# Performance work log

Measured on AMD Instinct MI355X. Metric: run time of the kernel, lower is better.

Reference implementation:

```python
import jax, jax.numpy as jnp
import numpy as np

C_IMG, C_TXT, NHEAD = 256, 768, 8
B, D, H, W, L = 8, 24, 24, 24, 77

def setup_inputs() -> dict:
    key = jax.random.key(0)
    ks = jax.random.split(key, 16)
    s = 0.02
    x_img = jax.random.normal(ks[0], (B, C_IMG, D, H, W), jnp.float32)
    x_txt = jax.random.normal(ks[1], (B, L, C_TXT), jnp.float32)
    # realistic padding: each sample has a valid length in [40, 77); True = padded key
    lengths = jax.random.randint(ks[2], (B,), 40, L)
    txt_mask = jnp.arange(L)[None, :] >= lengths[:, None]  # [B, L] bool
    inp = {
        "x_img": x_img,
        "x_txt": x_txt,
        "txt_mask": txt_mask,
        "q_proj_w": jax.random.normal(ks[3], (C_IMG, C_IMG), jnp.float32) * s,   # Conv3d 1x1, no bias
        "k_proj_w": jax.random.normal(ks[4], (C_IMG, C_TXT), jnp.float32) * s,   # Linear, no bias
        "v_proj_w": jax.random.normal(ks[5], (C_IMG, C_TXT), jnp.float32) * s,
        "in_q_w": jax.random.normal(ks[6], (C_IMG, C_IMG), jnp.float32) * s,     # MHA in_proj (q/k/v)
        "in_q_b": jnp.zeros((C_IMG,), jnp.float32),
        "in_k_w": jax.random.normal(ks[7], (C_IMG, C_IMG), jnp.float32) * s,
        "in_k_b": jnp.zeros((C_IMG,), jnp.float32),
        "in_v_w": jax.random.normal(ks[8], (C_IMG, C_IMG), jnp.float32) * s,
        "in_v_b": jnp.zeros((C_IMG,), jnp.float32),
        "out_proj_w": jax.random.normal(ks[9], (C_IMG, C_IMG), jnp.float32) * s, # MHA out_proj
        "out_proj_b": jnp.zeros((C_IMG,), jnp.float32),
        "out_conv_w": jax.random.normal(ks[10], (C_IMG, C_IMG), jnp.float32) * s, # self.out Conv3d 1x1 (bias)
        "out_conv_b": jnp.zeros((C_IMG,), jnp.float32),
        "norm_w": jnp.ones((C_IMG,), jnp.float32),  # InstanceNorm3d affine
        "norm_b": jnp.zeros((C_IMG,), jnp.float32),
    }
    return inp

def reference(x_img, x_txt, txt_mask, q_proj_w, k_proj_w, v_proj_w,
              in_q_w, in_q_b, in_k_w, in_k_b, in_v_w, in_v_b,
              out_proj_w, out_proj_b, out_conv_w, out_conv_b, norm_w, norm_b):
    Bq, C, d, h, w = x_img.shape
    N = d * h * w
    hd = C // NHEAD
    # q_proj (1x1 conv == channel matmul), flatten to tokens
    q = jnp.einsum('bcdhw,oc->bodhw', x_img, q_proj_w).reshape(Bq, C, N).transpose(0, 2, 1)  # [B,N,C]
    k = jnp.einsum('blt,ct->blc', x_txt, k_proj_w)  # [B,L,C]
    v = jnp.einsum('blt,ct->blc', x_txt, v_proj_w)
    # MHA internal projections
    qh = (q @ in_q_w.T + in_q_b).reshape(Bq, N, NHEAD, hd).transpose(0, 2, 1, 3)  # [B,h,N,hd]
    kh = (k @ in_k_w.T + in_k_b).reshape(Bq, -1, NHEAD, hd).transpose(0, 2, 1, 3)  # [B,h,L,hd]
    vh = (v @ in_v_w.T + in_v_b).reshape(Bq, -1, NHEAD, hd).transpose(0, 2, 1, 3)
    scores = jnp.einsum('bhnd,bhld->bhnl', qh, kh) / jnp.sqrt(jnp.asarray(hd, qh.dtype))
    neg = jnp.finfo(scores.dtype).min
    scores = jnp.where(txt_mask[:, None, None, :], neg, scores)
    attn = jax.nn.softmax(scores, axis=-1)  # [B,h,N,L]
    o = jnp.einsum('bhnl,bhld->bhnd', attn, vh).transpose(0, 2, 1, 3).reshape(Bq, N, C)
    o = o @ out_proj_w.T + out_proj_b
    o = o.transpose(0, 2, 1).reshape(Bq, C, d, h, w)
    # self.out 1x1 conv with bias
    o = jnp.einsum('bcdhw,oc->bodhw', o, out_conv_w) + out_conv_b[None, :, None, None, None]
    # residual + InstanceNorm3d(affine) + SiLU
    r = o + x_img
    mu = r.mean(axis=(2, 3, 4), keepdims=True)
    var = r.var(axis=(2, 3, 4), keepdims=True)
    xn = (r - mu) * jax.lax.rsqrt(var + 1e-5)
    out = jax.nn.silu(xn * norm_w[None, :, None, None, None] + norm_b[None, :, None, None, None])
    return out
```

## Files before the change

kernel.cpp:

```cpp
#include <hip/hip_runtime.h>
#include <cstdint>
#include <cstddef>

#define B_    8
#define CI    256
#define NH    8
#define HD    32
#define LQ    77
#define LP    80
#define NSP   13824
#define NTILE 216
#define SCALE 0.17677669529663687f

typedef float    float4_ __attribute__((ext_vector_type(4)));
typedef _Float16 half4_  __attribute__((ext_vector_type(4)));

#define MFMA16(a,b,c) __builtin_amdgcn_mfma_f32_16x16x16f16((a),(b),(c),0,0,0)

#define OFF_WQP  0
#define OFF_WOP  32768
#define OFF_WKP  65536
#define OFF_WVP  163840
#define OFF_KP   262144
#define OFF_VP   344064
#define OFF_BO   425984
#define OFF_IQBS 426240
#define OFF_AM   426496
#define OFF_STAT 427136

__global__ __launch_bounds__(256) void prep_kernel(
    const float* __restrict__ opb, const float* __restrict__ ocw,
    const float* __restrict__ ocb, const float* __restrict__ iqb,
    const void*  __restrict__ mask_in, float* __restrict__ ws)
{
    int blk = blockIdx.x, tid = threadIdx.x;
    if (blk == 0) {
        float a = ocb[tid];
        const float* row = ocw + tid * 256;
        #pragma unroll 4
        for (int m = 0; m < 256; ++m) a = fmaf(row[m], opb[m], a);
        ws[OFF_BO + tid] = a;
        ws[OFF_IQBS + tid] = iqb[tid] * SCALE;
    } else if (blk == 1) {
        __shared__ int s_is8;
        if (tid == 0) s_is8 = 0;
        __syncthreads();
        const unsigned char* m8 = (const unsigned char*)mask_in;
        for (int i = tid; i < B_ * LQ; i += 256)
            if ((i & 3) && m8[i]) atomicExch(&s_is8, 1);
        __syncthreads();
        int is8 = s_is8;
        const int* mi = (const int*)mask_in;
        float* mo = ws + OFF_AM;
        for (int i = tid; i < B_ * LP; i += 256) {
            int b = i / LP, l = i % LP;
            int v = 1;
            if (l < LQ) v = is8 ? (int)m8[b * LQ + l] : mi[b * LQ + l];
            mo[i] = v ? -1e30f : 0.0f;
        }
    } else {
        for (int i = tid; i < B_ * CI * 2; i += 256) ws[OFF_STAT + i] = 0.f;
    }
}

__global__ __launch_bounds__(256) void wcomb_kernel(
    const float* __restrict__ qpw, const float* __restrict__ iqw,
    const float* __restrict__ opw, const float* __restrict__ ocw,
    const float* __restrict__ kpw, const float* __restrict__ ikw,
    const float* __restrict__ vpw, const float* __restrict__ ivw,
    float* __restrict__ ws)
{
    int blk = blockIdx.x, tid = threadIdx.x;
    int lane = tid & 63, w = tid >> 6, g = lane >> 4, li = lane & 15;

    const float *iw, *pw; _Float16* dst; int pstride, ctb, otb; float scale = 1.f;
    if (blk < 16) {
        iw = iqw; pw = qpw; pstride = 256; dst = (_Float16*)(ws + OFF_WQP);
        ctb = blk >> 2; otb = blk & 3; scale = SCALE;
    } else if (blk < 32) {
        int j = blk - 16;
        iw = ocw; pw = opw; pstride = 256; dst = (_Float16*)(ws + OFF_WOP);
        ctb = j >> 2; otb = j & 3;
    } else if (blk < 80) {
        int j = blk - 32;
        iw = ikw; pw = kpw; pstride = 768; dst = (_Float16*)(ws + OFF_WKP);
        ctb = j >> 2; otb = j & 3;
    } else {
        int j = blk - 80;
        iw = ivw; pw = vpw; pstride = 768; dst = (_Float16*)(ws + OFF_WVP);
        ctb = j >> 2; otb = j & 3;
    }
    int ct = ctb * 4 + w;

    float4_ acc[4];
    #pragma unroll
    for (int i = 0; i < 4; ++i)
        #pragma unroll
        for (int r = 0; r < 4; ++r) acc[i][r] = 0.f;

    for (int mt = 0; mt < 16; ++mt) {
        half4_ ah;
        #pragma unroll
        for (int j = 0; j < 4; ++j)
            ah[j] = (_Float16)pw[(size_t)(mt * 16 + 4 * g + j) * pstride + ct * 16 + li];
        #pragma unroll
        for (int i = 0; i < 4; ++i) {
            int o = (otb * 4 + i) * 16 + li;
            float4_ bw = *(const float4_*)&iw[(size_t)o * 256 + mt * 16 + 4 * g];
            half4_ bh;
            #pragma unroll
            for (int j = 0; j < 4; ++j) bh[j] = (_Float16)bw[j];
            acc[i] = MFMA16(ah, bh, acc[i]);
        }
    }
    #pragma unroll
    for (int i = 0; i < 4; ++i) {
        half4_ oh;
        #pragma unroll
        for (int r = 0; r < 4; ++r) oh[r] = (_Float16)(acc[i][r] * scale);
        *(half4_*)&dst[((size_t)(ct * 16 + otb * 4 + i) * 64 + lane) * 4] = oh;
    }
}

__global__ __launch_bounds__(256) void kv_kernel(
    const float* __restrict__ xtxt, float* __restrict__ ws,
    const float* __restrict__ ikb, const float* __restrict__ ivb)
{
    const _Float16* wkA = (const _Float16*)(ws + OFF_WKP);
    const _Float16* wvA = (const _Float16*)(ws + OFF_WVP);
    _Float16* kp = (_Float16*)(ws + OFF_KP);
    _Float16* vp = (_Float16*)(ws + OFF_VP);

    int b = blockIdx.x >> 1, part = blockIdx.x & 1;
    int tid = threadIdx.x, lane = tid & 63, w = tid >> 6, g = lane >> 4, li = lane & 15;

    float4_ acc[4][5];
    if (part == 0) {
        #pragma unroll
        for (int i = 0; i < 4; ++i) {
            float4_ bias = *(const float4_*)&ikb[(w * 4 + i) * 16 + 4 * g];
            #pragma unroll
            for (int lt = 0; lt < 5; ++lt) acc[i][lt] = bias;
        }
    } else {
        #pragma unroll
        for (int i = 0; i < 4; ++i) {
            float bv = ivb[(w * 4 + i) * 16 + li];
            #pragma unroll
            for (int lt = 0; lt < 5; ++lt)
                #pragma unroll
                for (int r = 0; r < 4; ++r) acc[i][lt][r] = bv;
        }
    }

    for (int kt = 0; kt < 48; ++kt) {
        half4_ xh[5];
        #pragma unroll
        for (int lt = 0; lt < 5; ++lt) {
            int l = lt * 16 + li;
            float4_ xv = {0.f, 0.f, 0.f, 0.f};
            if (l < LQ)
                xv = *(const float4_*)&xtxt[(size_t)(b * LQ + l) * 768 + kt * 16 + 4 * g];
            #pragma unroll
            for (int j = 0; j < 4; ++j) xh[lt][j] = (_Float16)xv[j];
        }
        if (part == 0) {
            #pragma unroll
            for (int i = 0; i < 4; ++i) {
                half4_ aw = *(const half4_*)&wkA[((size_t)(kt * 16 + w * 4 + i) * 64 + lane) * 4];
                #pragma unroll
                for (int lt = 0; lt < 5; ++lt)
                    acc[i][lt] = MFMA16(aw, xh[lt], acc[i][lt]);
            }
        } else {
            #pragma unroll
            for (int i = 0; i < 4; ++i) {
                half4_ bw = *(const half4_*)&wvA[((size_t)(kt * 16 + w * 4 + i) * 64 + lane) * 4];
                #pragma unroll
                for (int lt = 0; lt < 5; ++lt)
                    acc[i][lt] = MFMA16(xh[lt], bw, acc[i][lt]);
            }
        }
    }

    #pragma unroll
    for (int i = 0; i < 4; ++i) {
        int ot = w * 4 + i, h = ot >> 1;
        size_t hb = (size_t)(b * NH + h) * 10;
        #pragma unroll
        for (int lt = 0; lt < 5; ++lt) {
            half4_ oh;
            #pragma unroll
            for (int r = 0; r < 4; ++r) oh[r] = (_Float16)acc[i][lt][r];
            if (part == 0) {
                int kd = ot & 1;
                *(half4_*)&kp[(hb + lt * 2 + kd) * 256 + lane * 4] = oh;
            } else {
                int dt = ot & 1;
                *(half4_*)&vp[(hb + dt * 5 + lt) * 256 + lane * 4] = oh;
            }
        }
    }
}

__global__ __launch_bounds__(256, 3) void main_kernel(
    const float* __restrict__ x_img, const float* __restrict__ ws,
    float* __restrict__ rout, float* __restrict__ stat)
{
    const _Float16* wqpk = (const _Float16*)(ws + OFF_WQP);
    const _Float16* wopk = (const _Float16*)(ws + OFF_WOP);
    const _Float16* kpck = (const _Float16*)(ws + OFF_KP);
    const _Float16* vpck = (const _Float16*)(ws + OFF_VP);
    const float* iqbs = ws + OFF_IQBS;
    const float* bog  = ws + OFF_BO;

    __shared__ _Float16 sh0[16384];
    __shared__ float am_s[LP];

    const int tid  = threadIdx.x;
    const int lane = tid & 63;
    const int w    = __builtin_amdgcn_readfirstlane(tid >> 6);
    const int g    = lane >> 4;
    const int li   = lane & 15;
    const int by   = blockIdx.y;
    const int n0   = blockIdx.x * 64;

    const float* xba = x_img + (size_t)by * CI * NSP + n0;
    float*       rba = rout  + (size_t)by * CI * NSP + n0;

    if (tid < LP) am_s[tid] = ws[OFF_AM + by * LP + tid];

    {
        int t = tid & 63, tf_s = t >> 4, tl = t & 15;
        for (int it = 0; it < 16; ++it) {
            int cbase = it * 16 + 4 * w;
            half4_ hv;
            #pragma unroll
            for (int j = 0; j < 4; ++j)
                hv[j] = (_Float16)xba[(size_t)(cbase + j) * NSP + t];
            *(half4_*)&sh0[((it * 4 + tf_s) * 64 + tl + 16 * w) * 4] = hv;
        }
    }
    __syncthreads();

    half4_ qh_h[4][4];
    {
        float4_ acc[4][4];
        #pragma unroll
        for (int of = 0; of < 4; ++of) {
            float4_ bias = *(const float4_*)&iqbs[w * 64 + of * 16 + 4 * g];
            #pragma unroll
            for (int tf = 0; tf < 4; ++tf) acc[of][tf] = bias;
        }
        for (int kt = 0; kt < 16; ++kt) {
            half4_ bfr[4], afr[4];
            #pragma unroll
            for (int tf = 0; tf < 4; ++tf)
                bfr[tf] = *(const half4_*)&sh0[((kt * 4 + tf) * 64 + lane) * 4];
            #pragma unroll
            for (int of = 0; of < 4; ++of)
                afr[of] = *(const half4_*)&wqpk[((size_t)(kt * 16 + w * 4 + of) * 64 + lane) * 4];
            #pragma unroll
            for (int of = 0; of < 4; ++of)
                #pragma unroll
                for (int tf = 0; tf < 4; ++tf)
                    acc[of][tf] = MFMA16(afr[of], bfr[tf], acc[of][tf]);
        }
        #pragma unroll
        for (int of = 0; of < 4; ++of)
            #pragma unroll
            for (int tf = 0; tf < 4; ++tf)
                #pragma unroll
                for (int r = 0; r < 4; ++r)
                    qh_h[of][tf][r] = (_Float16)acc[of][tf][r];
    }
    __syncthreads();

    #pragma unroll
    for (int hh = 0; hh < 2; ++hh) {
        const int h = 2 * w + hh;
        const _Float16* kp = kpck + (size_t)(by * NH + h) * 2560;
        const _Float16* vp = vpck + (size_t)(by * NH + h) * 2560;
        float mk[5][4];
        #pragma unroll
        for (int lt = 0; lt < 5; ++lt)
            #pragma unroll
            for (int r = 0; r < 4; ++r) mk[lt][r] = am_s[lt * 16 + 4 * g + r];
        #pragma unroll
        for (int tfh = 0; tfh < 2; ++tfh) {
            float4_ sc[5][2];
            #pragma unroll
            for (int lt = 0; lt < 5; ++lt)
                #pragma unroll
                for (int t2 = 0; t2 < 2; ++t2)
                    #pragma unroll
                    for (int r = 0; r < 4; ++r) sc[lt][t2][r] = 0.f;
            #pragma unroll
            for (int lt = 0; lt < 5; ++lt)
                #pragma unroll
                for (int kd = 0; kd < 2; ++kd) {
                    half4_ akf = *(const half4_*)&kp[((lt * 2 + kd) * 64 + lane) * 4];
                    #pragma unroll
                    for (int t2 = 0; t2 < 2; ++t2)
                        sc[lt][t2] = MFMA16(akf, qh_h[2 * hh + kd][tfh * 2 + t2], sc[lt][t2]);
                }
            #pragma unroll
            for (int lt = 0; lt < 5; ++lt)
                #pragma unroll
                for (int t2 = 0; t2 < 2; ++t2)
                    #pragma unroll
                    for (int r = 0; r < 4; ++r) sc[lt][t2][r] += mk[lt][r];
            float inv[2];
            #pragma unroll
            for (int t2 = 0; t2 < 2; ++t2) {
                float m = -3.0e38f;
                #pragma unroll
                for (int lt = 0; lt < 5; ++lt)
                    #pragma unroll
                    for (int r = 0; r < 4; ++r) m = fmaxf(m, sc[lt][t2][r]);
                m = fmaxf(m, __shfl_xor(m, 16));
                m = fmaxf(m, __shfl_xor(m, 32));
                float s = 0.f;
                #pragma unroll
                for (int lt = 0; lt < 5; ++lt)
                    #pragma unroll
                    for (int r = 0; r < 4; ++r) {
                        float e = __expf(sc[lt][t2][r] - m);
                        sc[lt][t2][r] = e;
                        s += e;
                    }
                s += __shfl_xor(s, 16);
                s += __shfl_xor(s, 32);
                inv[t2] = 1.0f / s;
            }
            float4_ oa[2][2];
            #pragma unroll
            for (int dt = 0; dt < 2; ++dt)
                #pragma unroll
                for (int t2 = 0; t2 < 2; ++t2)
                    #pragma unroll
                    for (int r = 0; r < 4; ++r) oa[dt][t2][r] = 0.f;
            #pragma unroll
            for (int lt = 0; lt < 5; ++lt) {
                half4_ pl[2];
                #pragma unroll
                for (int t2 = 0; t2 < 2; ++t2)
                    #pragma unroll
                    for (int r = 0; r < 4; ++r) pl[t2][r] = (_Float16)sc[lt][t2][r];
                #pragma unroll
                for (int dt = 0; dt < 2; ++dt) {
                    half4_ avf = *(const half4_*)&vp[((dt * 5 + lt) * 64 + lane) * 4];
                    #pragma unroll
                    for (int t2 = 0; t2 < 2; ++t2)
                        oa[dt][t2] = MFMA16(avf, pl[t2], oa[dt][t2]);
                }
            }
            #pragma unroll
            for (int dt = 0; dt < 2; ++dt)
                #pragma unroll
                for (int t2 = 0; t2 < 2; ++t2) {
                    half4_ ov;
                    #pragma unroll
                    for (int r = 0; r < 4; ++r) ov[r] = (_Float16)(oa[dt][t2][r] * inv[t2]);
                    *(half4_*)&sh0[(((h * 2 + dt) * 4 + tfh * 2 + t2) * 64 + lane) * 4] = ov;
                }
        }
    }
    __syncthreads();

    float4_ fa[4][4];
    #pragma unroll
    for (int of = 0; of < 4; ++of) {
        float4_ bias = *(const float4_*)&bog[w * 64 + of * 16 + 4 * g];
        #pragma unroll
        for (int tf = 0; tf < 4; ++tf) fa[of][tf] = bias;
    }
    for (int kt = 0; kt < 16; ++kt) {
        half4_ bfr[4], afr[4];
        #pragma unroll
        for (int tf = 0; tf < 4; ++tf)
            bfr[tf] = *(const half4_*)&sh0[((kt * 4 + tf) * 64 + lane) * 4];
        #pragma unroll
        for (int of = 0; of < 4; ++of)
            afr[of] = *(const half4_*)&wopk[((size_t)(kt * 16 + w * 4 + of) * 64 + lane) * 4];
        #pragma unroll
        for (int of = 0; of < 4; ++of)
            #pragma unroll
            for (int tf = 0; tf < 4; ++tf)
                fa[of][tf] = MFMA16(afr[of], bfr[tf], fa[of][tf]);
    }
    __syncthreads();

    #pragma unroll
    for (int of = 0; of < 4; ++of)
        #pragma unroll
        for (int tf = 0; tf < 4; ++tf)
            #pragma unroll
            for (int r = 0; r < 4; ++r) {
                int row = w * 64 + of * 16 + 4 * g + r;
                int q   = tf * 4 + (li >> 2);
                int qs  = q ^ (4 * g + r);
                sh0[row * 64 + qs * 4 + (li & 3)] = (_Float16)fa[of][tf][r];
            }
    __syncthreads();

    for (int it = 0; it < 16; ++it) {
        int flat = it * 256 + tid;
        int row = flat >> 4, q = flat & 15;
        half4_ hv = *(const half4_*)&sh0[row * 64 + ((q ^ (row & 15)) << 2)];
        float4_ xres = *(const float4_*)&xba[(size_t)row * NSP + q * 4];
        float4_ y;
        float s = 0.f, s2 = 0.f;
        #pragma unroll
        for (int e = 0; e < 4; ++e) {
            y[e] = (float)hv[e] + xres[e];
            s += y[e];
            s2 = fmaf(y[e], y[e], s2);
        }
        *(float4_*)&rba[(size_t)row * NSP + q * 4] = y;
        #pragma unroll
        for (int off = 1; off < 16; off <<= 1) {
            s  += __shfl_xor(s, off);
            s2 += __shfl_xor(s2, off);
        }
        if ((tid & 15) == 0) {
            atomicAdd(&stat[(by * CI + row) * 2],     s);
            atomicAdd(&stat[(by * CI + row) * 2 + 1], s2);
        }
    }
}

__global__ __launch_bounds__(256) void norm_kernel(
    float* __restrict__ rout, const float* __restrict__ nw,
    const float* __restrict__ nb, const float* __restrict__ stat)
{
    int blk = blockIdx.x;
    int c = blk & 255;
    float S  = stat[blk * 2];
    float S2 = stat[blk * 2 + 1];
    float mu = S * (1.0f / (float)NSP);
    float var = S2 * (1.0f / (float)NSP) - mu * mu;
    float rstd = rsqrtf(var + 1e-5f);
    float gg = nw[c] * rstd;
    float b2 = fmaf(-mu, gg, nb[c]);
    float4_* row4 = (float4_*)(rout + (size_t)blk * NSP);
    for (int i = threadIdx.x; i < NSP / 4; i += 256) {
        float4_ v = row4[i];
        #pragma unroll
        for (int u = 0; u < 4; ++u) {
            float y = fmaf(v[u], gg, b2);
            v[u] = y / (1.f + __expf(-y));
        }
        row4[i] = v;
    }
}

extern "C" void kernel_launch(void* const* d_in, const int* in_sizes, int n_in,
                              void* d_out, int out_size, void* d_ws, size_t ws_size,
                              hipStream_t stream) {
    const float* x_img = (const float*)d_in[0];
    const float* x_txt = (const float*)d_in[1];
    const void*  tmask = d_in[2];
    const float* qpw   = (const float*)d_in[3];
    const float* kpw   = (const float*)d_in[4];
    const float* vpw   = (const float*)d_in[5];
    const float* iqw   = (const float*)d_in[6];
    const float* iqb   = (const float*)d_in[7];
    const float* ikw   = (const float*)d_in[8];
    const float* ikb   = (const float*)d_in[9];
    const float* ivw   = (const float*)d_in[10];
    const float* ivb   = (const float*)d_in[11];
    const float* opw   = (const float*)d_in[12];
    const float* opb   = (const float*)d_in[13];
    const float* ocw   = (const float*)d_in[14];
    const float* ocb   = (const float*)d_in[15];
    const float* nw    = (const float*)d_in[16];
    const float* nb    = (const float*)d_in[17];
    float* ws  = (float*)d_ws;
    float* out = (float*)d_out;

    prep_kernel<<<3, 256, 0, stream>>>(opb, ocw, ocb, iqb, tmask, ws);
    wcomb_kernel<<<128, 256, 0, stream>>>(qpw, iqw, opw, ocw, kpw, ikw, vpw, ivw, ws);
    kv_kernel<<<16, 256, 0, stream>>>(x_txt, ws, ikb, ivb);
    main_kernel<<<dim3(NTILE, B_), 256, 0, stream>>>(x_img, ws, out, ws + OFF_STAT);
    norm_kernel<<<B_ * CI, 256, 0, stream>>>(out, nw, nb, ws + OFF_STAT);
}
```

Baseline: 504.6 us.

## Move instance-norm statistics from atomics into norm kernel and merge prep launch

Removes the per-tile atomicAdd accumulation of channel sums in main_kernel. norm_kernel now computes mean and variance itself with an extra read pass over each channel row, which eliminates atomic contention and the stat-zeroing step. The prep work is folded into wcomb_kernel as two extra blocks, saving one launch. Main_kernel also switches to coalesced float4 loads when staging x_img and raises its occupancy hint from 3 to 4 blocks, at the cost of an extra full read of the output in norm_kernel.

Result: faster. 460.3 us (-8.8%).

```diff
diff --git a/kernel.cpp b/kernel.cpp
--- a/kernel.cpp
+++ b/kernel.cpp
@@ -26,53 +26,48 @@
 #define OFF_BO   425984
 #define OFF_IQBS 426240
 #define OFF_AM   426496
-#define OFF_STAT 427136
-
-__global__ __launch_bounds__(256) void prep_kernel(
-    const float* __restrict__ opb, const float* __restrict__ ocw,
-    const float* __restrict__ ocb, const float* __restrict__ iqb,
-    const void*  __restrict__ mask_in, float* __restrict__ ws)
-{
-    int blk = blockIdx.x, tid = threadIdx.x;
-    if (blk == 0) {
-        float a = ocb[tid];
-        const float* row = ocw + tid * 256;
-        #pragma unroll 4
-        for (int m = 0; m < 256; ++m) a = fmaf(row[m], opb[m], a);
-        ws[OFF_BO + tid] = a;
-        ws[OFF_IQBS + tid] = iqb[tid] * SCALE;
-    } else if (blk == 1) {
-        __shared__ int s_is8;
-        if (tid == 0) s_is8 = 0;
-        __syncthreads();
-        const unsigned char* m8 = (const unsigned char*)mask_in;
-        for (int i = tid; i < B_ * LQ; i += 256)
-            if ((i & 3) && m8[i]) atomicExch(&s_is8, 1);
-        __syncthreads();
-        int is8 = s_is8;
-        const int* mi = (const int*)mask_in;
-        float* mo = ws + OFF_AM;
-        for (int i = tid; i < B_ * LP; i += 256) {
-            int b = i / LP, l = i % LP;
-            int v = 1;
-            if (l < LQ) v = is8 ? (int)m8[b * LQ + l] : mi[b * LQ + l];
-            mo[i] = v ? -1e30f : 0.0f;
-        }
-    } else {
-        for (int i = tid; i < B_ * CI * 2; i += 256) ws[OFF_STAT + i] = 0.f;
-    }
-}
 
 __global__ __launch_bounds__(256) void wcomb_kernel(
     const float* __restrict__ qpw, const float* __restrict__ iqw,
     const float* __restrict__ opw, const float* __restrict__ ocw,
     const float* __restrict__ kpw, const float* __restrict__ ikw,
     const float* __restrict__ vpw, const float* __restrict__ ivw,
+    const float* __restrict__ opb, const float* __restrict__ ocb,
+    const float* __restrict__ iqb, const void* __restrict__ mask_in,
     float* __restrict__ ws)
 {
     int blk = blockIdx.x, tid = threadIdx.x;
+
+    if (blk >= 128) {
+        if (blk == 128) {
+            float a = ocb[tid];
+            const float* row = ocw + tid * 256;
+            #pragma unroll 4
+            for (int m = 0; m < 256; ++m) a = fmaf(row[m], opb[m], a);
+            ws[OFF_BO + tid] = a;
+            ws[OFF_IQBS + tid] = iqb[tid] * SCALE;
+        } else {
+            __shared__ int s_is8;
+            if (tid == 0) s_is8 = 0;
+            __syncthreads();
+            const unsigned char* m8 = (const unsigned char*)mask_in;
+            for (int i = tid; i < B_ * LQ; i += 256)
+                if ((i & 3) && m8[i]) atomicExch(&s_is8, 1);
+            __syncthreads();
+            int is8 = s_is8;
+            const int* mi = (const int*)mask_in;
+            float* mo = ws + OFF_AM;
+            for (int i = tid; i < B_ * LP; i += 256) {
+                int b = i / LP, l = i % LP;
+                int v = 1;
+                if (l < LQ) v = is8 ? (int)m8[b * LQ + l] : mi[b * LQ + l];
+                mo[i] = v ? -1e30f : 0.0f;
+            }
+        }
+        return;
+    }
+
     int lane = tid & 63, w = tid >> 6, g = lane >> 4, li = lane & 15;
-
     const float *iw, *pw; _Float16* dst; int pstride, ctb, otb; float scale = 1.f;
     if (blk < 16) {
         iw = iqw; pw = qpw; pstride = 256; dst = (_Float16*)(ws + OFF_WQP);
@@ -203,9 +198,9 @@
     }
 }
 
-__global__ __launch_bounds__(256, 3) void main_kernel(
+__global__ __launch_bounds__(256, 4) void main_kernel(
     const float* __restrict__ x_img, const float* __restrict__ ws,
-    float* __restrict__ rout, float* __restrict__ stat)
+    float* __restrict__ rout)
 {
     const _Float16* wqpk = (const _Float16*)(ws + OFF_WQP);
     const _Float16* wopk = (const _Float16*)(ws + OFF_WOP);
@@ -223,22 +218,23 @@
     const int g    = lane >> 4;
     const int li   = lane & 15;
     const int by   = blockIdx.y;
-    const int n0   = blockIdx.x * 64;
+    const int bx   = blockIdx.x;
+    const int n0   = bx * 64;
 
     const float* xba = x_img + (size_t)by * CI * NSP + n0;
     float*       rba = rout  + (size_t)by * CI * NSP + n0;
 
     if (tid < LP) am_s[tid] = ws[OFF_AM + by * LP + tid];
 
-    {
-        int t = tid & 63, tf_s = t >> 4, tl = t & 15;
-        for (int it = 0; it < 16; ++it) {
-            int cbase = it * 16 + 4 * w;
-            half4_ hv;
-            #pragma unroll
-            for (int j = 0; j < 4; ++j)
-                hv[j] = (_Float16)xba[(size_t)(cbase + j) * NSP + t];
-            *(half4_*)&sh0[((it * 4 + tf_s) * 64 + tl + 16 * w) * 4] = hv;
+    for (int it = 0; it < 16; ++it) {
+        int idx = it * 256 + tid;
+        int c = idx >> 4, t4 = (idx & 15) * 4;
+        float4_ xv = *(const float4_*)&xba[(size_t)c * NSP + t4];
+        int kt = c >> 4, lhi = 16 * ((c >> 2) & 3), jj = c & 3;
+        #pragma unroll
+        for (int u = 0; u < 4; ++u) {
+            int t = t4 + u;
+            sh0[((kt * 4 + (t >> 4)) * 64 + (t & 15) + lhi) * 4 + jj] = (_Float16)xv[u];
         }
     }
     __syncthreads();
@@ -410,41 +406,50 @@
         half4_ hv = *(const half4_*)&sh0[row * 64 + ((q ^ (row & 15)) << 2)];
         float4_ xres = *(const float4_*)&xba[(size_t)row * NSP + q * 4];
         float4_ y;
-        float s = 0.f, s2 = 0.f;
-        #pragma unroll
-        for (int e = 0; e < 4; ++e) {
-            y[e] = (float)hv[e] + xres[e];
-            s += y[e];
-            s2 = fmaf(y[e], y[e], s2);
-        }
+        #pragma unroll
+        for (int e = 0; e < 4; ++e) y[e] = (float)hv[e] + xres[e];
         *(float4_*)&rba[(size_t)row * NSP + q * 4] = y;
-        #pragma unroll
-        for (int off = 1; off < 16; off <<= 1) {
-            s  += __shfl_xor(s, off);
-            s2 += __shfl_xor(s2, off);
-        }
-        if ((tid & 15) == 0) {
-            atomicAdd(&stat[(by * CI + row) * 2],     s);
-            atomicAdd(&stat[(by * CI + row) * 2 + 1], s2);
-        }
     }
 }
 
 __global__ __launch_bounds__(256) void norm_kernel(
-    float* __restrict__ rout, const float* __restrict__ nw,
-    const float* __restrict__ nb, const float* __restrict__ stat)
+    float* __restrict__ rout, const float* __restrict__ nw, const float* __restrict__ nb)
 {
+    __shared__ float red[8];
+    __shared__ float stats[2];
     int blk = blockIdx.x;
     int c = blk & 255;
-    float S  = stat[blk * 2];
-    float S2 = stat[blk * 2 + 1];
-    float mu = S * (1.0f / (float)NSP);
-    float var = S2 * (1.0f / (float)NSP) - mu * mu;
-    float rstd = rsqrtf(var + 1e-5f);
+    float* row = rout + (size_t)blk * NSP;
+    float4_* row4 = (float4_*)row;
+    int tid = threadIdx.x;
+
+    float s = 0.f, s2 = 0.f;
+    for (int i = tid; i < NSP / 4; i += 256) {
+        float4_ v = row4[i];
+        #pragma unroll
+        for (int u = 0; u < 4; ++u) { s += v[u]; s2 = fmaf(v[u], v[u], s2); }
+    }
+    #pragma unroll
+    for (int off = 32; off > 0; off >>= 1) {
+        s  += __shfl_down(s, off);
+        s2 += __shfl_down(s2, off);
+    }
+    int wv = tid >> 6, ln = tid & 63;
+    if (ln == 0) { red[wv] = s; red[4 + wv] = s2; }
+    __syncthreads();
+    if (tid == 0) {
+        float S  = red[0] + red[1] + red[2] + red[3];
+        float S2 = red[4] + red[5] + red[6] + red[7];
+        float mu = S * (1.0f / (float)NSP);
+        float var = S2 * (1.0f / (float)NSP) - mu * mu;
+        stats[0] = mu;
+        stats[1] = rsqrtf(var + 1e-5f);
+    }
+    __syncthreads();
+    float mu = stats[0], rstd = stats[1];
     float gg = nw[c] * rstd;
     float b2 = fmaf(-mu, gg, nb[c]);
-    float4_* row4 = (float4_*)(rout + (size_t)blk * NSP);
-    for (int i = threadIdx.x; i < NSP / 4; i += 256) {
+    for (int i = tid; i < NSP / 4; i += 256) {
         float4_ v = row4[i];
         #pragma unroll
         for (int u = 0; u < 4; ++u) {
@@ -479,9 +484,9 @@
     float* ws  = (float*)d_ws;
     float* out = (float*)d_out;
 
-    prep_kernel<<<3, 256, 0, stream>>>(opb, ocw, ocb, iqb, tmask, ws);
-    wcomb_kernel<<<128, 256, 0, stream>>>(qpw, iqw, opw, ocw, kpw, ikw, vpw, ivw, ws);
+    wcomb_kernel<<<130, 256, 0, stream>>>(qpw, iqw, opw, ocw, kpw, ikw, vpw, ivw,
+                                          opb, ocb, iqb, tmask, ws);
     kv_kernel<<<16, 256, 0, stream>>>(x_txt, ws, ikb, ivb);
-    main_kernel<<<dim3(NTILE, B_), 256, 0, stream>>>(x_img, ws, out, ws + OFF_STAT);
-    norm_kernel<<<B_ * CI, 256, 0, stream>>>(out, nw, nb, ws + OFF_STAT);
+    main_kernel<<<dim3(NTILE, B_), 256, 0, stream>>>(x_img, ws, out);
+    norm_kernel<<<B_ * CI, 256, 0, stream>>>(out, nw, nb);
 }
```
